# Optimization experiments

Measured on AMD Instinct MI355X. Metric: run time of the kernel, lower is better.

The kernel has to match this reference:

```python
import jax, jax.numpy as jnp
import numpy as np

B, S, E, D = 256, 256, 2, 128  # batch, seq_len, encoder_dim, decoder_dim


def setup_inputs() -> dict:
    key = jax.random.key(0)
    ks = jax.random.split(key, 9)
    u = lambda k, shape, n: jax.random.uniform(k, shape, jnp.float32, -1.0 / np.sqrt(n), 1.0 / np.sqrt(n))
    return {
        "out_encoder": jax.random.normal(ks[0], (B, S, E), jnp.float32),
        "W1_w": u(ks[1], (S, S), S),            # Linear(seq_len, seq_len)
        "W1_b": u(ks[2], (S,), S),
        "W2_w": u(ks[3], (S, 2 * S), 2 * S),    # Linear(2*seq_len, seq_len)
        "W2_b": u(ks[4], (S,), 2 * S),
        "W_ih": u(ks[5], (4 * D, E), D),        # LSTMCell input weights (i,f,g,o)
        "W_hh": u(ks[6], (4 * D, D), D),
        "b_ih": u(ks[7], (4 * D,), D),
        "b_hh": u(ks[8], (4 * D,), D),
    }


def reference(out_encoder, W1_w, W1_b, W2_w, W2_b, W_ih, W_hh, b_ih, b_hh):
    b, s, e = out_encoder.shape
    d = W_hh.shape[1]
    dt = out_encoder.dtype

    # W_2 term: encoder flattened to [B, 2S]; identical every step, hoist it.
    w2term = out_encoder.reshape(b, s * e) @ W2_w.T + W2_b          # [B, S]
    # W_1 applied to a row of S copies of h_d equals h_d * rowsum(W1) + b.
    w1sum = W1_w.sum(axis=1)                                        # [S]

    def attn(h):  # h: [B, D] -> context [B, E]
        hterm = h[:, :, None] * w1sum[None, None, :] + W1_b         # [B, D, S]
        en = jnp.tanh(w2term[:, None, :] + hterm)                   # [B, D, S]
        alpha = jax.nn.softmax(en, axis=-1).mean(axis=1)            # [B, S] (softmax over seq)
        return jnp.einsum('bs,bse->be', alpha, out_encoder)         # [B, E]

    def lstm_cell(x, h, c):
        gates = x @ W_ih.T + h @ W_hh.T + b_ih + b_hh               # [B, 4D]
        i, f, g, o = jnp.split(gates, 4, axis=-1)
        c = jax.nn.sigmoid(f) * c + jax.nn.sigmoid(i) * jnp.tanh(g)
        h = jax.nn.sigmoid(o) * jnp.tanh(c)
        return h, c

    h0 = jnp.zeros((b, d), dt)
    c0 = jnp.zeros((b, d), dt)

    def step(carry, _):
        h, c = carry
        x = attn(h)
        h, c = lstm_cell(x, h, c)
        return (h, c), h

    _, hs = jax.lax.scan(step, (h0, c0), None, length=s)
    return hs  # [S, B, D]: stacked decoder hidden states (original returns a list of h_t)
```

## Files before the change

### kernel.cpp

```cpp
#include <hip/hip_runtime.h>

#define NB 256
#define NS 256
#define NE 2
#define ND 128
#define NT 512
#define NN 16
#define RING 32
#define SLOT 144
#define SLOTH 160

typedef float vf4 __attribute__((ext_vector_type(4)));
typedef _Float16 f16x8 __attribute__((ext_vector_type(8)));
typedef float f32x4 __attribute__((ext_vector_type(4)));

constexpr float L2E = 1.4426950408889634f;
constexpr float PI_F = 3.14159265358979323846f;

__device__ const float CT[16][16] = {
 {1,0,0,0,0,0,0,0,0,0,0,0,0,0,0,0},
 {0,1,0,0,0,0,0,0,0,0,0,0,0,0,0,0},
 {-1,0,2,0,0,0,0,0,0,0,0,0,0,0,0,0},
 {0,-3,0,4,0,0,0,0,0,0,0,0,0,0,0,0},
 {1,0,-8,0,8,0,0,0,0,0,0,0,0,0,0,0},
 {0,5,0,-20,0,16,0,0,0,0,0,0,0,0,0,0},
 {-1,0,18,0,-48,0,32,0,0,0,0,0,0,0,0,0},
 {0,-7,0,56,0,-112,0,64,0,0,0,0,0,0,0,0},
 {1,0,-32,0,160,0,-256,0,128,0,0,0,0,0,0,0},
 {0,9,0,-120,0,432,0,-576,0,256,0,0,0,0,0,0},
 {-1,0,50,0,-400,0,1120,0,-1280,0,512,0,0,0,0,0},
 {0,-11,0,220,0,-1232,0,2816,0,-2816,0,1024,0,0,0,0},
 {1,0,-72,0,840,0,-3584,0,6912,0,-6144,0,2048,0,0,0},
 {0,13,0,-364,0,2912,0,-9984,0,16640,0,-13312,0,4096,0,0},
 {-1,0,98,0,-1568,0,9408,0,-26880,0,39424,0,-28672,0,8192,0},
 {0,-15,0,560,0,-6048,0,28800,0,-70400,0,92160,0,-61440,0,16384}};

template <int C>
__device__ __forceinline__ float dppadd(float x) {
    return x + __builtin_bit_cast(float,
        __builtin_amdgcn_update_dpp(0, __builtin_bit_cast(int, x), C, 0xF, 0xF, true));
}
__device__ __forceinline__ float red_quad(float x) {
    x = dppadd<0xB1>(x); x = dppadd<0x4E>(x); return x;
}
__device__ __forceinline__ float red_oct(float x) {
    x = dppadd<0xB1>(x); x = dppadd<0x4E>(x); x = dppadd<0x141>(x); return x;
}
__device__ __forceinline__ float red_wave64(float x) {
    x = dppadd<0xB1>(x); x = dppadd<0x4E>(x); x = dppadd<0x141>(x);
    x = dppadd<0x140>(x); x = dppadd<0x142>(x); x = dppadd<0x143>(x); return x;
}
__device__ __forceinline__ float red_half32(float x) {
    x = dppadd<0xB1>(x); x = dppadd<0x4E>(x); x = dppadd<0x141>(x);
    x = dppadd<0x140>(x); x = dppadd<0x142>(x); return x;
}
__device__ __forceinline__ float red_grp16(float x) {
    x = dppadd<0x141>(x); x = dppadd<0x140>(x);
    x = dppadd<0x142>(x); x = dppadd<0x143>(x); return x;
}

__global__ __launch_bounds__(NT, 2)
void attn_lstm_decoder(const float* __restrict__ enc,
                       const float* __restrict__ W1w,
                       const float* __restrict__ W1b,
                       const float* __restrict__ W2w,
                       const float* __restrict__ W2b,
                       const float* __restrict__ Wih,
                       const float* __restrict__ Whh,
                       const float* __restrict__ bih,
                       const float* __restrict__ bhh,
                       float* __restrict__ out)
{
    const int b    = blockIdx.x;
    const int t    = threadIdx.x;
    const int wave = t >> 6;
    const int lane = t & 63;
    const int g    = t >> 2;
    const int q    = t & 3;
    const bool qb0 = q & 1;
    const bool qb1 = q & 2;
    const int grp  = lane >> 4;
    const int nib  = lane & 15;
    const int half = lane >> 5;
    const int idx  = lane & 31;
    const int jnode = 2 * wave + half;

    __shared__ __align__(16) float    hist[RING * SLOT];
    __shared__ __align__(16) _Float16 hist16[RING * SLOTH];
    __shared__ __align__(16) float xwbuf[2][16];
    __shared__ __align__(16) float gbuf[4 * ND];
    __shared__ float A2_l[NS];
    __shared__ float g2_l[NS];
    __shared__ float e0_l[NS];
    __shared__ float e1_l[NS];
    __shared__ float Ml[NN * NN];
    __shared__ float2 Pn[NN];
    __shared__ float2 Vl[NN];
    __shared__ float Pm0[NN], Pm1[NN];

    {
        float v = enc[b * (NS * NE) + t];
        if (t & 1) e1_l[t >> 1] = v; else e0_l[t >> 1] = v;
    }
    if (t < NN * NN) {
        const int mi = t >> 4, mj = t & 15;
        const float w = (mi == 0) ? (1.0f / NN) : (2.0f / NN);
        Ml[t] = w * __cosf((float)(mi * (2 * mj + 1)) * (PI_F / (2 * NN)));
    }
    __syncthreads();

    for (int r = 0; r < 32; ++r) {
        const int s = wave * 32 + r;
        float p = W1w[s * NS + lane]       + W1w[s * NS + lane + 64]
                + W1w[s * NS + lane + 128] + W1w[s * NS + lane + 192];
        p = red_wave64(p);
        if (lane == 63) g2_l[s] = p * (2.0f * L2E);
        float qq = 0.0f;
        #pragma unroll
        for (int kk = 0; kk < 8; ++kk) {
            const int c = lane + kk * 64;
            const float ev = (c & 1) ? e1_l[c >> 1] : e0_l[c >> 1];
            qq = fmaf(ev, W2w[s * (2 * NS) + c], qq);
        }
        qq = red_wave64(qq);
        if (lane == 63) A2_l[s] = (qq + W2b[s] + W1b[s]) * (2.0f * L2E);
    }
    __syncthreads();

    {
        const float y  = __cosf((float)(2 * jnode + 1) * (PI_F / (2 * NN)));
        const float C2 = -2.0f * L2E;
        float l = 0.0f, p0 = 0.0f, p1 = 0.0f;
        #pragma unroll
        for (int k = 0; k < 8; ++k) {
            const int s = k * 32 + idx;
            const float m1 = fmaf(y, g2_l[s], A2_l[s]);
            const float u  = __builtin_amdgcn_exp2f(m1);
            const float rc = __builtin_amdgcn_rcpf(u + 1.0f);
            const float e  = __builtin_amdgcn_exp2f(rc * C2);
            l += e;
            p0 = fmaf(e, e0_l[s], p0);
            p1 = fmaf(e, e1_l[s], p1);
        }
        l = red_half32(l); p0 = red_half32(p0); p1 = red_half32(p1);
        if ((lane & 31) == 31) {
            const float rl = __builtin_amdgcn_rcpf(l);
            Pn[jnode] = make_float2(p0 * rl, p1 * rl);
        }
    }
    __syncthreads();

    if (t < NN) {
        float v0 = 0.0f, v1 = 0.0f;
        #pragma unroll
        for (int j = 0; j < NN; ++j) {
            v0 = fmaf(Ml[t * NN + j], Pn[j].x, v0);
            v1 = fmaf(Ml[t * NN + j], Pn[j].y, v1);
        }
        Vl[t] = make_float2(v0 * (1.0f / ND), v1 * (1.0f / ND));
    }

    f16x8 wf[4][4];
    float wi0_[4], wi1_[4], bb_[4];
    #pragma unroll
    for (int rt = 0; rt < 4; ++rt) {
        const int row = 64 * wave + 16 * rt + nib;
        #pragma unroll
        for (int kt = 0; kt < 4; ++kt) {
            const vf4 wa = *reinterpret_cast<const vf4*>(Whh + row * ND + 32 * kt + 8 * grp);
            const vf4 wb = *reinterpret_cast<const vf4*>(Whh + row * ND + 32 * kt + 8 * grp + 4);
            f16x8 wv;
            wv[0] = (_Float16)wa.x; wv[1] = (_Float16)wa.y;
            wv[2] = (_Float16)wa.z; wv[3] = (_Float16)wa.w;
            wv[4] = (_Float16)wb.x; wv[5] = (_Float16)wb.y;
            wv[6] = (_Float16)wb.z; wv[7] = (_Float16)wb.w;
            wf[rt][kt] = wv;
        }
    }
    #pragma unroll
    for (int j = 0; j < 4; ++j) {
        const int r = g + 128 * j;
        wi0_[j] = Wih[r * 2 + 0];
        wi1_[j] = Wih[r * 2 + 1];
        bb_[j]  = bih[r] + bhh[r];
    }

    if (t < ND) {
        hist[31 * SLOT + 36 * (t >> 5) + (t & 31)] = 0.0f;
        hist16[31 * SLOTH + 40 * (t >> 5) + (t & 31)] = (_Float16)0.0f;
    }
    float h_reg = 0.0f, c_reg = 0.0f;
    __syncthreads();

    if (t < NN) {
        float s0 = 0.0f, s1 = 0.0f;
        #pragma unroll
        for (int k = 0; k < NN; ++k) {
            s0 = fmaf(Vl[k].x, CT[k][t], s0);
            s1 = fmaf(Vl[k].y, CT[k][t], s1);
        }
        Pm0[t] = s0; Pm1[t] = s1;
    }
    __syncthreads();

    float Q0[4], Q1[4];
    #pragma unroll
    for (int i = 0; i < 4; ++i) { Q0[i] = Pm0[4 * i + q]; Q1[i] = Pm1[4 * i + q]; }

    auto phaseG = [&](float h, int pw) {
        const float h2 = h * h;
        const float h3 = h2 * h;
        const float h4 = h2 * h2;
        const float hq = qb1 ? (qb0 ? h3 : h2) : (qb0 ? h : 1.0f);
        float a0 = fmaf(Q0[3], h4, Q0[2]);
        a0 = fmaf(a0, h4, Q0[1]);
        a0 = fmaf(a0, h4, Q0[0]);
        float a1 = fmaf(Q1[3], h4, Q1[2]);
        a1 = fmaf(a1, h4, Q1[1]);
        a1 = fmaf(a1, h4, Q1[0]);
        a0 *= hq;
        a1 *= hq;
        a0 = red_quad(a0);  a1 = red_quad(a1);
        a0 = red_grp16(a0); a1 = red_grp16(a1);
        if (lane == 63) {
            xwbuf[pw][2 * wave + 0] = a0;
            xwbuf[pw][2 * wave + 1] = a1;
        }
    };

    phaseG(0.0f, 0);
    __syncthreads();

    for (int step = 0; step < NS; ++step) {
        const int pr = step & 1;
        const int rs = (step + RING - 1) & (RING - 1);
        const int ws = step & (RING - 1);

        f16x8 af[4];
        const _Float16* hsl = &hist16[rs * SLOTH + 8 * grp];
        #pragma unroll
        for (int kt = 0; kt < 4; ++kt)
            af[kt] = __builtin_bit_cast(f16x8,
                *reinterpret_cast<const int4*>(hsl + 40 * kt));

        f32x4 acc[4];
        #pragma unroll
        for (int rt = 0; rt < 4; ++rt) {
            f32x4 a = {0.0f, 0.0f, 0.0f, 0.0f};
            #pragma unroll
            for (int kt = 0; kt < 4; ++kt)
                a = __builtin_amdgcn_mfma_f32_16x16x32_f16(af[kt], wf[rt][kt], a, 0, 0, 0);
            acc[rt] = a;
        }
        if (lane < 16) {
            #pragma unroll
            for (int rt = 0; rt < 4; ++rt) {
                const int r = 64 * wave + 16 * rt + lane;
                gbuf[((r & 127) << 2) | (r >> 7)] = acc[rt][0];
            }
        }
        __syncthreads();

        float2 xv = *reinterpret_cast<const float2*>(&xwbuf[pr][2 * (lane & 7)]);
        const f32x4 gv = *reinterpret_cast<const f32x4*>(&gbuf[g << 2]);

        if ((step & 15) == 0 && step > 0) {
            const int sb  = (step - 16) & (RING - 1);
            const int k   = t >> 5;
            const int l32 = t & 31;
            const int w   = 4 * l32;
            const vf4 v = *reinterpret_cast<const vf4*>(
                &hist[(sb + k) * SLOT + 36 * (w >> 5) + (w & 31)]);
            *reinterpret_cast<vf4*>(
                &out[(size_t)(step - 16 + k) * (NB * ND) + b * ND + w]) = v;
        }

        float x0 = red_oct(xv.x);
        float x1 = red_oct(xv.y);

        const float gi = gv[0] + fmaf(x0, wi0_[0], fmaf(x1, wi1_[0], bb_[0]));
        const float gf = gv[1] + fmaf(x0, wi0_[1], fmaf(x1, wi1_[1], bb_[1]));
        const float gg = gv[2] + fmaf(x0, wi0_[2], fmaf(x1, wi1_[2], bb_[2]));
        const float go = gv[3] + fmaf(x0, wi0_[3], fmaf(x1, wi1_[3], bb_[3]));

        const float si = __builtin_amdgcn_rcpf(1.0f + __builtin_amdgcn_exp2f(-L2E * gi));
        const float sf = __builtin_amdgcn_rcpf(1.0f + __builtin_amdgcn_exp2f(-L2E * gf));
        const float so = __builtin_amdgcn_rcpf(1.0f + __builtin_amdgcn_exp2f(-L2E * go));
        const float tg = 1.0f - 2.0f * __builtin_amdgcn_rcpf(__builtin_amdgcn_exp2f(2.0f * L2E * gg) + 1.0f);
        c_reg = sf * c_reg + si * tg;
        const float tc2 = 1.0f - 2.0f * __builtin_amdgcn_rcpf(__builtin_amdgcn_exp2f(2.0f * L2E * c_reg) + 1.0f);
        h_reg = so * tc2;

        if (q == 0) {
            hist[ws * SLOT + 36 * (g >> 5) + (g & 31)] = h_reg;
            hist16[ws * SLOTH + 40 * (g >> 5) + (g & 31)] = (_Float16)h_reg;
        }
        phaseG(h_reg, pr ^ 1);

        __syncthreads();
    }

    {
        const int k   = t >> 5;
        const int l32 = t & 31;
        const int w   = 4 * l32;
        const vf4 v = *reinterpret_cast<const vf4*>(
            &hist[(16 + k) * SLOT + 36 * (w >> 5) + (w & 31)]);
        *reinterpret_cast<vf4*>(
            &out[(size_t)(240 + k) * (NB * ND) + b * ND + w]) = v;
    }
}

extern "C" void kernel_launch(void* const* d_in, const int* in_sizes, int n_in,
                              void* d_out, int out_size, void* d_ws, size_t ws_size,
                              hipStream_t stream) {
    const float* enc = (const float*)d_in[0];
    const float* W1w = (const float*)d_in[1];
    const float* W1b = (const float*)d_in[2];
    const float* W2w = (const float*)d_in[3];
    const float* W2b = (const float*)d_in[4];
    const float* Wih = (const float*)d_in[5];
    const float* Whh = (const float*)d_in[6];
    const float* bih = (const float*)d_in[7];
    const float* bhh = (const float*)d_in[8];
    attn_lstm_decoder<<<NB, NT, 0, stream>>>(enc, W1w, W1b, W2w, W2b,
                                             Wih, Whh, bih, bhh, (float*)d_out);
}
```

Baseline: 303.7 us.

## Keep LSTM gate exchange in-wave via bpermute, dropping per-step LDS barrier

W_hh rows are remapped so each wave's MFMAs produce all four gates for its own 16 hidden units. The gate values then reach the right lanes through ds_bpermute instead of a shared gbuf buffer, which removes one block-wide __syncthreads per recurrent step. Each quad lane now evaluates a single sigmoid or tanh for its own gate and shares the result with DPP quad broadcasts, replacing four transcendentals per lane. One CT table row loses a trailing literal zero, which leaves its value unchanged because missing elements are zero-initialised.

```diff
diff --git a/kernel.cpp b/kernel.cpp
--- a/kernel.cpp
+++ b/kernel.cpp
@@ -27,7 +27,7 @@
  {-1,0,18,0,-48,0,32,0,0,0,0,0,0,0,0,0},
  {0,-7,0,56,0,-112,0,64,0,0,0,0,0,0,0,0},
  {1,0,-32,0,160,0,-256,0,128,0,0,0,0,0,0,0},
- {0,9,0,-120,0,432,0,-576,0,256,0,0,0,0,0,0},
+ {0,9,0,-120,0,432,0,-576,0,256,0,0,0,0,0},
  {-1,0,50,0,-400,0,1120,0,-1280,0,512,0,0,0,0,0},
  {0,-11,0,220,0,-1232,0,2816,0,-2816,0,1024,0,0,0,0},
  {1,0,-72,0,840,0,-3584,0,6912,0,-6144,0,2048,0,0,0},
@@ -38,6 +38,11 @@
 template <int C>
 __device__ __forceinline__ float dppadd(float x) {
     return x + __builtin_bit_cast(float,
+        __builtin_amdgcn_update_dpp(0, __builtin_bit_cast(int, x), C, 0xF, 0xF, true));
+}
+template <int C>
+__device__ __forceinline__ float quadbc(float x) {
+    return __builtin_bit_cast(float,
         __builtin_amdgcn_update_dpp(0, __builtin_bit_cast(int, x), C, 0xF, 0xF, true));
 }
 __device__ __forceinline__ float red_quad(float x) {
@@ -88,7 +93,6 @@
     __shared__ __align__(16) float    hist[RING * SLOT];
     __shared__ __align__(16) _Float16 hist16[RING * SLOTH];
     __shared__ __align__(16) float xwbuf[2][16];
-    __shared__ __align__(16) float gbuf[4 * ND];
     __shared__ float A2_l[NS];
     __shared__ float g2_l[NS];
     __shared__ float e0_l[NS];
@@ -161,10 +165,9 @@
     }
 
     f16x8 wf[4][4];
-    float wi0_[4], wi1_[4], bb_[4];
     #pragma unroll
     for (int rt = 0; rt < 4; ++rt) {
-        const int row = 64 * wave + 16 * rt + nib;
+        const int row = 128 * rt + 16 * wave + nib;
         #pragma unroll
         for (int kt = 0; kt < 4; ++kt) {
             const vf4 wa = *reinterpret_cast<const vf4*>(Whh + row * ND + 32 * kt + 8 * grp);
@@ -177,13 +180,14 @@
             wf[rt][kt] = wv;
         }
     }
-    #pragma unroll
-    for (int j = 0; j < 4; ++j) {
-        const int r = g + 128 * j;
-        wi0_[j] = Wih[r * 2 + 0];
-        wi1_[j] = Wih[r * 2 + 1];
-        bb_[j]  = bih[r] + bhh[r];
-    }
+    const int rq = 128 * q + g;
+    const float wiq0 = Wih[rq * 2 + 0];
+    const float wiq1 = Wih[rq * 2 + 1];
+    const float bbq  = bih[rq] + bhh[rq];
+    const float sA  = (q == 2) ? (2.0f * L2E) : (-L2E);
+    const float cA1 = (q == 2) ? -2.0f : 1.0f;
+    const float cA0 = (q == 2) ? 1.0f : 0.0f;
+    const int bidx = ((((lane & 3) << 4) | (lane >> 2)) << 2);
 
     if (t < ND) {
         hist[31 * SLOT + 36 * (t >> 5) + (t & 31)] = 0.0f;
@@ -243,26 +247,7 @@
             af[kt] = __builtin_bit_cast(f16x8,
                 *reinterpret_cast<const int4*>(hsl + 40 * kt));
 
-        f32x4 acc[4];
-        #pragma unroll
-        for (int rt = 0; rt < 4; ++rt) {
-            f32x4 a = {0.0f, 0.0f, 0.0f, 0.0f};
-            #pragma unroll
-            for (int kt = 0; kt < 4; ++kt)
-                a = __builtin_amdgcn_mfma_f32_16x16x32_f16(af[kt], wf[rt][kt], a, 0, 0, 0);
-            acc[rt] = a;
-        }
-        if (lane < 16) {
-            #pragma unroll
-            for (int rt = 0; rt < 4; ++rt) {
-                const int r = 64 * wave + 16 * rt + lane;
-                gbuf[((r & 127) << 2) | (r >> 7)] = acc[rt][0];
-            }
-        }
-        __syncthreads();
-
         float2 xv = *reinterpret_cast<const float2*>(&xwbuf[pr][2 * (lane & 7)]);
-        const f32x4 gv = *reinterpret_cast<const f32x4*>(&gbuf[g << 2]);
 
         if ((step & 15) == 0 && step > 0) {
             const int sb  = (step - 16) & (RING - 1);
@@ -278,17 +263,33 @@
         float x0 = red_oct(xv.x);
         float x1 = red_oct(xv.y);
 
-        const float gi = gv[0] + fmaf(x0, wi0_[0], fmaf(x1, wi1_[0], bb_[0]));
-        const float gf = gv[1] + fmaf(x0, wi0_[1], fmaf(x1, wi1_[1], bb_[1]));
-        const float gg = gv[2] + fmaf(x0, wi0_[2], fmaf(x1, wi1_[2], bb_[2]));
-        const float go = gv[3] + fmaf(x0, wi0_[3], fmaf(x1, wi1_[3], bb_[3]));
-
-        const float si = __builtin_amdgcn_rcpf(1.0f + __builtin_amdgcn_exp2f(-L2E * gi));
-        const float sf = __builtin_amdgcn_rcpf(1.0f + __builtin_amdgcn_exp2f(-L2E * gf));
-        const float so = __builtin_amdgcn_rcpf(1.0f + __builtin_amdgcn_exp2f(-L2E * go));
-        const float tg = 1.0f - 2.0f * __builtin_amdgcn_rcpf(__builtin_amdgcn_exp2f(2.0f * L2E * gg) + 1.0f);
-        c_reg = sf * c_reg + si * tg;
-        const float tc2 = 1.0f - 2.0f * __builtin_amdgcn_rcpf(__builtin_amdgcn_exp2f(2.0f * L2E * c_reg) + 1.0f);
+        f32x4 acc[4];
+        #pragma unroll
+        for (int rt = 0; rt < 4; ++rt) {
+            f32x4 a = {0.0f, 0.0f, 0.0f, 0.0f};
+            #pragma unroll
+            for (int kt = 0; kt < 4; ++kt)
+                a = __builtin_amdgcn_mfma_f32_16x16x32_f16(af[kt], wf[rt][kt], a, 0, 0, 0);
+            acc[rt] = a;
+        }
+
+        const float a01 = (lane & 16) ? acc[1][0] : acc[0][0];
+        const float a23 = (lane & 16) ? acc[3][0] : acc[2][0];
+        const float av  = (lane & 32) ? a23 : a01;
+        const float myg = __builtin_bit_cast(float,
+            __builtin_amdgcn_ds_bpermute(bidx, __builtin_bit_cast(int, av)));
+
+        const float gq  = myg + fmaf(x0, wiq0, fmaf(x1, wiq1, bbq));
+        const float act = fmaf(cA1,
+            __builtin_amdgcn_rcpf(1.0f + __builtin_amdgcn_exp2f(sA * gq)), cA0);
+        const float si = quadbc<0x00>(act);
+        const float sf = quadbc<0x55>(act);
+        const float tg = quadbc<0xAA>(act);
+        const float so = quadbc<0xFF>(act);
+
+        c_reg = fmaf(sf, c_reg, si * tg);
+        const float tc2 = 1.0f - 2.0f * __builtin_amdgcn_rcpf(
+            __builtin_amdgcn_exp2f(2.0f * L2E * c_reg) + 1.0f);
         h_reg = so * tc2;
 
         if (q == 0) {
```

New measurement: 261.5 us (median of 3 runs). 1.16x faster.

## Remap LSTM gate rows per wave to drop gate exchange and one barrier

Applied to the files above, without the earlier changes.

Reassigns W_hh rows so each wave computes all four gates (i,f,g,o) for its own 16 hidden units. The gate pre-activations then stay in registers, which removes the shared gbuf exchange and one block-wide barrier per recurrent step. The h history ring shrinks to a double buffer, and each step's h is stored straight to global memory instead of being flushed in batches of 16. The MFMA chain is split into two independent accumulators, and __syncthreads is replaced by an explicit lgkmcnt wait plus s_barrier. The cost is many small strided global stores and a hand-written barrier sequence that has to stay correct.

```diff
diff --git a/kernel.cpp b/kernel.cpp
--- a/kernel.cpp
+++ b/kernel.cpp
@@ -6,8 +6,6 @@
 #define ND 128
 #define NT 512
 #define NN 16
-#define RING 32
-#define SLOT 144
 #define SLOTH 160
 
 typedef float vf4 __attribute__((ext_vector_type(4)));
@@ -27,7 +25,7 @@
  {-1,0,18,0,-48,0,32,0,0,0,0,0,0,0,0,0},
  {0,-7,0,56,0,-112,0,64,0,0,0,0,0,0,0,0},
  {1,0,-32,0,160,0,-256,0,128,0,0,0,0,0,0,0},
- {0,9,0,-120,0,432,0,-576,0,256,0,0,0,0,0,0},
+ {0,9,0,-120,0,432,0,-576,0,256,0,0,0,0,0},
  {-1,0,50,0,-400,0,1120,0,-1280,0,512,0,0,0,0,0},
  {0,-11,0,220,0,-1232,0,2816,0,-2816,0,1024,0,0,0,0},
  {1,0,-72,0,840,0,-3584,0,6912,0,-6144,0,2048,0,0,0},
@@ -40,9 +38,6 @@
     return x + __builtin_bit_cast(float,
         __builtin_amdgcn_update_dpp(0, __builtin_bit_cast(int, x), C, 0xF, 0xF, true));
 }
-__device__ __forceinline__ float red_quad(float x) {
-    x = dppadd<0xB1>(x); x = dppadd<0x4E>(x); return x;
-}
 __device__ __forceinline__ float red_oct(float x) {
     x = dppadd<0xB1>(x); x = dppadd<0x4E>(x); x = dppadd<0x141>(x); return x;
 }
@@ -53,10 +48,6 @@
 __device__ __forceinline__ float red_half32(float x) {
     x = dppadd<0xB1>(x); x = dppadd<0x4E>(x); x = dppadd<0x141>(x);
     x = dppadd<0x140>(x); x = dppadd<0x142>(x); return x;
-}
-__device__ __forceinline__ float red_grp16(float x) {
-    x = dppadd<0x141>(x); x = dppadd<0x140>(x);
-    x = dppadd<0x142>(x); x = dppadd<0x143>(x); return x;
 }
 
 __global__ __launch_bounds__(NT, 2)
@@ -75,20 +66,17 @@
     const int t    = threadIdx.x;
     const int wave = t >> 6;
     const int lane = t & 63;
-    const int g    = t >> 2;
-    const int q    = t & 3;
-    const bool qb0 = q & 1;
-    const bool qb1 = q & 2;
     const int grp  = lane >> 4;
     const int nib  = lane & 15;
+    const int gl   = 16 * wave + nib;
+    const bool qb0 = grp & 1;
+    const bool qb1 = grp & 2;
     const int half = lane >> 5;
     const int idx  = lane & 31;
     const int jnode = 2 * wave + half;
 
-    __shared__ __align__(16) float    hist[RING * SLOT];
-    __shared__ __align__(16) _Float16 hist16[RING * SLOTH];
+    __shared__ __align__(16) _Float16 hist16[2 * SLOTH];
     __shared__ __align__(16) float xwbuf[2][16];
-    __shared__ __align__(16) float gbuf[4 * ND];
     __shared__ float A2_l[NS];
     __shared__ float g2_l[NS];
     __shared__ float e0_l[NS];
@@ -161,10 +149,9 @@
     }
 
     f16x8 wf[4][4];
-    float wi0_[4], wi1_[4], bb_[4];
     #pragma unroll
     for (int rt = 0; rt < 4; ++rt) {
-        const int row = 64 * wave + 16 * rt + nib;
+        const int row = 128 * rt + 16 * wave + nib;
         #pragma unroll
         for (int kt = 0; kt < 4; ++kt) {
             const vf4 wa = *reinterpret_cast<const vf4*>(Whh + row * ND + 32 * kt + 8 * grp);
@@ -177,18 +164,16 @@
             wf[rt][kt] = wv;
         }
     }
+    float wi0_[4], wi1_[4], bb_[4];
     #pragma unroll
     for (int j = 0; j < 4; ++j) {
-        const int r = g + 128 * j;
+        const int r = 128 * j + gl;
         wi0_[j] = Wih[r * 2 + 0];
         wi1_[j] = Wih[r * 2 + 1];
         bb_[j]  = bih[r] + bhh[r];
     }
 
-    if (t < ND) {
-        hist[31 * SLOT + 36 * (t >> 5) + (t & 31)] = 0.0f;
-        hist16[31 * SLOTH + 40 * (t >> 5) + (t & 31)] = (_Float16)0.0f;
-    }
+    if (t < ND) hist16[SLOTH + 40 * (t >> 5) + (t & 31)] = (_Float16)0.0f;
     float h_reg = 0.0f, c_reg = 0.0f;
     __syncthreads();
 
@@ -205,7 +190,7 @@
 
     float Q0[4], Q1[4];
     #pragma unroll
-    for (int i = 0; i < 4; ++i) { Q0[i] = Pm0[4 * i + q]; Q1[i] = Pm1[4 * i + q]; }
+    for (int i = 0; i < 4; ++i) { Q0[i] = Pm0[4 * i + grp]; Q1[i] = Pm1[4 * i + grp]; }
 
     auto phaseG = [&](float h, int pw) {
         const float h2 = h * h;
@@ -220,8 +205,7 @@
         a1 = fmaf(a1, h4, Q1[0]);
         a0 *= hq;
         a1 *= hq;
-        a0 = red_quad(a0);  a1 = red_quad(a1);
-        a0 = red_grp16(a0); a1 = red_grp16(a1);
+        a0 = red_wave64(a0); a1 = red_wave64(a1);
         if (lane == 63) {
             xwbuf[pw][2 * wave + 0] = a0;
             xwbuf[pw][2 * wave + 1] = a1;
@@ -231,10 +215,12 @@
     phaseG(0.0f, 0);
     __syncthreads();
 
+    const int hoff = 40 * (gl >> 5) + (gl & 31);
+
     for (int step = 0; step < NS; ++step) {
         const int pr = step & 1;
-        const int rs = (step + RING - 1) & (RING - 1);
-        const int ws = step & (RING - 1);
+        const int rs = pr ^ 1;
+        const int ws = pr;
 
         f16x8 af[4];
         const _Float16* hsl = &hist16[rs * SLOTH + 8 * grp];
@@ -243,71 +229,49 @@
             af[kt] = __builtin_bit_cast(f16x8,
                 *reinterpret_cast<const int4*>(hsl + 40 * kt));
 
-        f32x4 acc[4];
+        float2 xv = *reinterpret_cast<const float2*>(&xwbuf[pr][2 * (lane & 7)]);
+        const float x0 = red_oct(xv.x);
+        const float x1 = red_oct(xv.y);
+        float bt[4];
+        #pragma unroll
+        for (int j = 0; j < 4; ++j)
+            bt[j] = fmaf(x0, wi0_[j], fmaf(x1, wi1_[j], bb_[j]));
+
+        float ga[4];
         #pragma unroll
         for (int rt = 0; rt < 4; ++rt) {
-            f32x4 a = {0.0f, 0.0f, 0.0f, 0.0f};
-            #pragma unroll
-            for (int kt = 0; kt < 4; ++kt)
-                a = __builtin_amdgcn_mfma_f32_16x16x32_f16(af[kt], wf[rt][kt], a, 0, 0, 0);
-            acc[rt] = a;
-        }
-        if (lane < 16) {
-            #pragma unroll
-            for (int rt = 0; rt < 4; ++rt) {
-                const int r = 64 * wave + 16 * rt + lane;
-                gbuf[((r & 127) << 2) | (r >> 7)] = acc[rt][0];
-            }
-        }
-        __syncthreads();
-
-        float2 xv = *reinterpret_cast<const float2*>(&xwbuf[pr][2 * (lane & 7)]);
-        const f32x4 gv = *reinterpret_cast<const f32x4*>(&gbuf[g << 2]);
-
-        if ((step & 15) == 0 && step > 0) {
-            const int sb  = (step - 16) & (RING - 1);
-            const int k   = t >> 5;
-            const int l32 = t & 31;
-            const int w   = 4 * l32;
-            const vf4 v = *reinterpret_cast<const vf4*>(
-                &hist[(sb + k) * SLOT + 36 * (w >> 5) + (w & 31)]);
-            *reinterpret_cast<vf4*>(
-                &out[(size_t)(step - 16 + k) * (NB * ND) + b * ND + w]) = v;
-        }
-
-        float x0 = red_oct(xv.x);
-        float x1 = red_oct(xv.y);
-
-        const float gi = gv[0] + fmaf(x0, wi0_[0], fmaf(x1, wi1_[0], bb_[0]));
-        const float gf = gv[1] + fmaf(x0, wi0_[1], fmaf(x1, wi1_[1], bb_[1]));
-        const float gg = gv[2] + fmaf(x0, wi0_[2], fmaf(x1, wi1_[2], bb_[2]));
-        const float go = gv[3] + fmaf(x0, wi0_[3], fmaf(x1, wi1_[3], bb_[3]));
+            f32x4 a0 = {0.0f, 0.0f, 0.0f, 0.0f};
+            f32x4 a1 = {0.0f, 0.0f, 0.0f, 0.0f};
+            a0 = __builtin_amdgcn_mfma_f32_16x16x32_f16(af[0], wf[rt][0], a0, 0, 0, 0);
+            a1 = __builtin_amdgcn_mfma_f32_16x16x32_f16(af[2], wf[rt][2], a1, 0, 0, 0);
+            a0 = __builtin_amdgcn_mfma_f32_16x16x32_f16(af[1], wf[rt][1], a0, 0, 0, 0);
+            a1 = __builtin_amdgcn_mfma_f32_16x16x32_f16(af[3], wf[rt][3], a1, 0, 0, 0);
+            ga[rt] = a0[0] + a1[0];
+        }
+
+        const float gi = ga[0] + bt[0];
+        const float gf = ga[1] + bt[1];
+        const float gg = ga[2] + bt[2];
+        const float go = ga[3] + bt[3];
 
         const float si = __builtin_amdgcn_rcpf(1.0f + __builtin_amdgcn_exp2f(-L2E * gi));
         const float sf = __builtin_amdgcn_rcpf(1.0f + __builtin_amdgcn_exp2f(-L2E * gf));
         const float so = __builtin_amdgcn_rcpf(1.0f + __builtin_amdgcn_exp2f(-L2E * go));
-        const float tg = 1.0f - 2.0f * __builtin_amdgcn_rcpf(__builtin_amdgcn_exp2f(2.0f * L2E * gg) + 1.0f);
-        c_reg = sf * c_reg + si * tg;
-        const float tc2 = 1.0f - 2.0f * __builtin_amdgcn_rcpf(__builtin_amdgcn_exp2f(2.0f * L2E * c_reg) + 1.0f);
+        const float tg = 1.0f - 2.0f * __builtin_amdgcn_rcpf(
+            __builtin_amdgcn_exp2f(2.0f * L2E * gg) + 1.0f);
+        c_reg = fmaf(sf, c_reg, si * tg);
+        const float tc2 = 1.0f - 2.0f * __builtin_amdgcn_rcpf(
+            __builtin_amdgcn_exp2f(2.0f * L2E * c_reg) + 1.0f);
         h_reg = so * tc2;
 
-        if (q == 0) {
-            hist[ws * SLOT + 36 * (g >> 5) + (g & 31)] = h_reg;
-            hist16[ws * SLOTH + 40 * (g >> 5) + (g & 31)] = (_Float16)h_reg;
+        if (grp == 0) {
+            hist16[ws * SLOTH + hoff] = (_Float16)h_reg;
+            out[(size_t)step * (NB * ND) + b * ND + gl] = h_reg;
         }
         phaseG(h_reg, pr ^ 1);
 
-        __syncthreads();
-    }
-
-    {
-        const int k   = t >> 5;
-        const int l32 = t & 31;
-        const int w   = 4 * l32;
-        const vf4 v = *reinterpret_cast<const vf4*>(
-            &hist[(16 + k) * SLOT + 36 * (w >> 5) + (w & 31)]);
-        *reinterpret_cast<vf4*>(
-            &out[(size_t)(240 + k) * (NB * ND) + b * ND + w]) = v;
+        asm volatile("s_waitcnt lgkmcnt(0)" ::: "memory");
+        __builtin_amdgcn_s_barrier();
     }
 }
 
```

Result: faster. 271.0 us (-10.8%).
